# Kernel tuning notes

Measured on AMD Instinct MI355X. Metric: run time of the kernel, lower is better.

## Reference

```python
import jax, jax.numpy as jnp
import numpy as np

H, KVH, P = 32, 8, 64          # heads, kv heads, head_dim (state dim n == P here)
GROUPS = H // KVH
D = H * P                      # hidden = 2048
CONV_DIM = (H + 2 * KVH) * P   # 3072
PROJ = (H + 2 * KVH + H) * P + H  # 5152
CHUNK = 128
EPS = 1e-5
B_, L_ = 2, 2048


def silu(x):
    return x * jax.nn.sigmoid(x)


def segsum(x):
    # x: [..., T] -> [..., T, T] with out[i, j] = sum_{j < k <= i} x[k], -inf above diag
    T = x.shape[-1]
    xb = jnp.broadcast_to(x[..., :, None], x.shape + (T,))
    strict = jnp.tril(jnp.ones((T, T), bool), -1)
    s = jnp.cumsum(jnp.where(strict, xb, 0.0), axis=-2)
    incl = jnp.tril(jnp.ones((T, T), bool))
    return jnp.where(incl, s, -jnp.inf)


def ssd(x, A, Bm, Cm, chunk):
    # Mamba2 chunked scan (SSD). x:[b,l,h,p] (already * dt), A:[b,l,h] (A*dt), B/C:[b,l,h,n]
    b, l, h, p = x.shape
    n = Bm.shape[-1]
    c = l // chunk
    x = x.reshape(b, c, chunk, h, p)
    Bm = Bm.reshape(b, c, chunk, h, n)
    Cm = Cm.reshape(b, c, chunk, h, n)
    A = A.reshape(b, c, chunk, h).transpose(0, 3, 1, 2)  # [b,h,c,l]
    Acs = jnp.cumsum(A, axis=-1)
    # intra-chunk (diagonal blocks)
    Lmat = jnp.exp(segsum(A))  # [b,h,c,l,l]
    Yd = jnp.einsum('bclhn,bcshn,bhcls,bcshp->bclhp', Cm, Bm, Lmat, x)
    # chunk-final states
    dstates = jnp.exp(Acs[..., -1:] - Acs)  # [b,h,c,l]
    states = jnp.einsum('bclhn,bhcl,bclhp->bchpn', Bm, dstates, x)
    states = jnp.concatenate([jnp.zeros_like(states[:, :1]), states], axis=1)
    dchunk = jnp.exp(segsum(jnp.pad(Acs[..., -1], ((0, 0), (0, 0), (1, 0)))))  # [b,h,c+1,c+1]
    states = jnp.einsum('bhzc,bchpn->bzhpn', dchunk, states)[:, :-1]
    # inter-chunk contribution
    Yo = jnp.einsum('bclhn,bchpn,bhcl->bclhp', Cm, states, jnp.exp(Acs))
    return (Yd + Yo).reshape(b, l, h, p)


def setup_inputs() -> dict:
    key = jax.random.key(0)
    ks = jax.random.split(key, 8)
    s = 0.02
    hidden_states = jax.random.normal(ks[0], (B_, L_, D), jnp.float32)
    W_vkqgdt = jax.random.normal(ks[1], (PROJ, D), jnp.float32) * s
    # conv init: identity tap on last position + small noise so grads are nontrivial
    conv_w = jnp.zeros((CONV_DIM, 2), jnp.float32).at[:, 1].set(1.0)
    conv_w = conv_w + jax.random.normal(ks[2], (CONV_DIM, 2), jnp.float32) * s
    conv_b = jax.random.normal(ks[3], (CONV_DIM,), jnp.float32) * s
    # dt_bias init as in the module: inverse-softplus of dt ~ LogUniform(1e-3, 1e-1)
    u = jax.random.uniform(ks[4], (H,), jnp.float32)
    dtv = jnp.exp(u * (np.log(0.1) - np.log(0.001)) + np.log(0.001))
    dtv = jnp.clip(dtv, 0.001)
    dt_bias = dtv + jnp.log(-jnp.expm1(-dtv))
    A_log_bias = jnp.zeros((H,), jnp.float32)
    gnorm_w = jnp.ones((P,), jnp.float32)
    W_o = jax.random.normal(ks[5], (D, D), jnp.float32) * s
    return {'hidden_states': hidden_states, 'W_vkqgdt': W_vkqgdt, 'conv_w': conv_w,
            'conv_b': conv_b, 'dt_bias': dt_bias, 'A_log_bias': A_log_bias,
            'gnorm_w': gnorm_w, 'W_o': W_o}


def reference(hidden_states, W_vkqgdt, conv_w, conv_b, dt_bias, A_log_bias, gnorm_w, W_o):
    b, l, _ = hidden_states.shape
    proj = hidden_states @ W_vkqgdt.T  # [b,l,PROJ]
    vkq, g, dt = jnp.split(proj, [CONV_DIM, CONV_DIM + H * P], axis=2)
    # causal depthwise conv (kernel=2) + SiLU
    x_prev = jnp.pad(vkq, ((0, 0), (1, 0), (0, 0)))[:, :-1]
    vkq = silu(x_prev * conv_w[:, 0] + vkq * conv_w[:, 1] + conv_b)
    v, k, q = jnp.split(vkq, [KVH * P, 2 * KVH * P], axis=2)
    v = jnp.repeat(v.reshape(b, l, KVH, P), GROUPS, axis=2)  # [b,l,H,P]
    k = jnp.repeat(k.reshape(b, l, KVH, P), GROUPS, axis=2)
    q = q.reshape(b, l, H, P)
    dt = jax.nn.softplus(dt + dt_bias)          # [b,l,H]
    A = -jnp.exp(A_log_bias.astype(jnp.float32))  # [H]
    y = ssd(v * dt[..., None], dt * A, k, q, CHUNK)  # x=v, B=k, C=q
    # fused RMSNorm + swish gate
    g = g.reshape(b, l, H, P)
    yn = y * jax.lax.rsqrt(jnp.mean(y * y, axis=-1, keepdims=True) + EPS) * gnorm_w
    y_true = (yn * silu(g)).reshape(b, l, D)
    return y_true @ W_o.T
```

## Files before the change

kernel.cpp:

```cpp
#include <hip/hip_runtime.h>
#include <hip/hip_bf16.h>
#include <math.h>

typedef __bf16 bf16;
typedef __bf16 bf16x4 __attribute__((ext_vector_type(4)));
typedef __bf16 bf16x8 __attribute__((ext_vector_type(8)));
typedef float f32x4 __attribute__((ext_vector_type(4)));

#define NB 2
#define LSEQ 2048
#define NH 32
#define NKVH 8
#define HD 64
#define DMODEL 2048
#define CONVD 3072
#define NPROJ 5152
#define NPADN 5248
#define NCHUNK 16
#define CHUNK 128
#define ROWS 4096
#define EPSF 1e-5f

__device__ __forceinline__ float fsilu(float x) { return x / (1.0f + __expf(-x)); }
__device__ __forceinline__ float fsoftplus(float raw) {
  return (raw > 20.0f) ? raw : log1pf(__expf(raw));
}

__device__ __forceinline__ void gld_lds16(const void* g, void* l) {
  __builtin_amdgcn_global_load_lds(
      (const __attribute__((address_space(1))) void*)g,
      (__attribute__((address_space(3))) void*)l, 16, 0, 0);
}

__device__ __forceinline__ bf16x8 lds_read_b128(const bf16* p) {
  bf16x8 r;
  unsigned off = (unsigned)(unsigned long)(__attribute__((address_space(3))) bf16*)p;
  asm volatile("ds_read_b128 %0, %1" : "=v"(r) : "v"(off));
  return r;
}
#define SBAR() asm volatile("s_barrier" ::: "memory")

__device__ __forceinline__ int swz64(int row, int col) {
  return row * 64 + ((((col >> 3) ^ row) & 7) << 3) + (col & 7);
}
__device__ __forceinline__ int swz128(int row, int col) {
  return row * 128 + (((col >> 3) ^ (row & 7)) << 3) + (col & 7);
}

__device__ __forceinline__ void stage64(const bf16* gsrc, bf16* lds, int tid, int nelem) {
  for (int i0 = 0; i0 < nelem; i0 += 2048) {
    int e = i0 + tid * 8;
    int row = e >> 6;
    int sc = ((tid & 7) ^ (row & 7)) << 3;
    gld_lds16((const void*)(gsrc + (row << 6) + sc), (void*)(lds + e));
  }
}
__device__ __forceinline__ void stage128(const bf16* gsrc, bf16* lds, int tid, int nelem) {
  for (int i0 = 0; i0 < nelem; i0 += 2048) {
    int e = i0 + tid * 8;
    int row = e >> 7;
    int sc = (((tid & 15) ^ (row & 7))) << 3;
    gld_lds16((const void*)(gsrc + (row << 7) + sc), (void*)(lds + e));
  }
}

__device__ __forceinline__ void stage_tileY(const bf16* g, bf16* l, int ldg, int tid) {
#pragma unroll
  for (int it = 0; it < 4; ++it) {
    int e = it * 2048 + tid * 8;
    int r = e >> 6;
    int sc = ((tid & 7) ^ (r & 7)) << 3;
    gld_lds16((const void*)(g + (long)r * ldg + sc), (void*)(l + e));
  }
}

__device__ __forceinline__ void wave_scan128(float& a0, float& a1, int lane) {
#pragma unroll
  for (int off = 1; off < 64; off <<= 1) {
    float t0 = __shfl_up(a0, off);
    float t1 = __shfl_up(a1, off);
    if (lane >= off) { a0 += t0; a1 += t1; }
  }
  a1 += __shfl(a0, 63);
}

__global__ __launch_bounds__(256) void cast_all_kernel(
    const float* __restrict__ hs, const float* __restrict__ w1, const float* __restrict__ wo,
    bf16* __restrict__ hs_b, bf16* __restrict__ w1_b, bf16* __restrict__ wo_b) {
  const long n1 = (long)ROWS * DMODEL / 8;
  const long n2 = (long)NPADN * DMODEL / 8;
  const long n3 = (long)DMODEL * DMODEL / 8;
  long total = n1 + n2 + n3;
  long stride = (long)gridDim.x * blockDim.x;
  for (long i = blockIdx.x * (long)blockDim.x + threadIdx.x; i < total; i += stride) {
    if (i < n1) {
      float4 v0 = ((const float4*)hs)[2 * i];
      float4 v1 = ((const float4*)hs)[2 * i + 1];
      ((bf16x8*)hs_b)[i] = bf16x8{(bf16)v0.x, (bf16)v0.y, (bf16)v0.z, (bf16)v0.w,
                                  (bf16)v1.x, (bf16)v1.y, (bf16)v1.z, (bf16)v1.w};
    } else if (i < n1 + n2) {
      long j = i - n1;
      int n = (int)((j * 8) >> 11);
      bf16x8 o = {};
      if (n < NPROJ) {
        float4 v0 = ((const float4*)w1)[2 * j];
        float4 v1 = ((const float4*)w1)[2 * j + 1];
        o = bf16x8{(bf16)v0.x, (bf16)v0.y, (bf16)v0.z, (bf16)v0.w,
                   (bf16)v1.x, (bf16)v1.y, (bf16)v1.z, (bf16)v1.w};
      }
      ((bf16x8*)w1_b)[j] = o;
    } else {
      long j = i - n1 - n2;
      float4 v0 = ((const float4*)wo)[2 * j];
      float4 v1 = ((const float4*)wo)[2 * j + 1];
      ((bf16x8*)wo_b)[j] = bf16x8{(bf16)v0.x, (bf16)v0.y, (bf16)v0.z, (bf16)v0.w,
                                  (bf16)v1.x, (bf16)v1.y, (bf16)v1.z, (bf16)v1.w};
    }
  }
}

template <typename OutT>
__global__ __launch_bounds__(256, 2) void gemm2p_kernel(
    const bf16* __restrict__ A, const bf16* __restrict__ B, OutT* __restrict__ C,
    int M, int N, int K, int ntx) {
  __shared__ __align__(16) bf16 As[2 * 128 * 64];
  __shared__ __align__(16) bf16 Bs[2 * 128 * 64];
  const int tid = threadIdx.x;
  const int lane = tid & 63;
  const int wave = tid >> 6;
  const int wm = wave >> 1, wn = wave & 1;

  const int GM = 8;
  int lid = blockIdx.x;
  {
    int nwg = gridDim.x;
    int xcd = lid & 7;
    int q = nwg >> 3, r = nwg & 7;
    lid = (xcd < r ? xcd * (q + 1) : r * (q + 1) + (xcd - r) * q) + (lid >> 3);
  }
  int group = GM * ntx;
  int gid = lid / group;
  int rem = lid - gid * group;
  int bm = gid * GM + (rem % GM);
  int bn = rem / GM;

  const bf16* Ag = A + (long)bm * 128 * K;
  const bf16* Bg = B + (long)bn * 128 * K;
  const int NT = K >> 6;

  const int fbA = (wm * 64 + (lane & 15)) * 64 + (((lane >> 4) ^ (lane & 7)) << 3);
  const int fbB = (wn * 64 + (lane & 15)) * 64 + (((lane >> 4) ^ (lane & 7)) << 3);

  f32x4 acc[4][4] = {};

  stage_tileY(Ag, As, K, tid);
  stage_tileY(Bg, Bs, K, tid);
  asm volatile("s_waitcnt vmcnt(0)" ::: "memory");
  SBAR();

  for (int t = 0; t < NT; ++t) {
    const int c = t & 1;
    const bf16* At = As + c * 8192;
    const bf16* Bt = Bs + c * 8192;
    if (t + 1 < NT) {
      stage_tileY(Ag + (t + 1) * 64, As + (c ^ 1) * 8192, K, tid);
      stage_tileY(Bg + (t + 1) * 64, Bs + (c ^ 1) * 8192, K, tid);
    }
    bf16x8 af[4][2], bf_[4][2];
#pragma unroll
    for (int mi = 0; mi < 4; ++mi)
#pragma unroll
      for (int ks = 0; ks < 2; ++ks)
        af[mi][ks] = lds_read_b128(At + ((fbA + mi * 1024) ^ (ks << 5)));
#pragma unroll
    for (int ni = 0; ni < 4; ++ni)
#pragma unroll
      for (int ks = 0; ks < 2; ++ks)
        bf_[ni][ks] = lds_read_b128(Bt + ((fbB + ni * 1024) ^ (ks << 5)));
    asm volatile("s_waitcnt lgkmcnt(0)" ::: "memory");
    __builtin_amdgcn_sched_barrier(0);
    __builtin_amdgcn_s_setprio(1);
#pragma unroll
    for (int mi = 0; mi < 4; ++mi)
#pragma unroll
      for (int ni = 0; ni < 4; ++ni)
#pragma unroll
        for (int ks = 0; ks < 2; ++ks)
          acc[mi][ni] = __builtin_amdgcn_mfma_f32_16x16x32_bf16(af[mi][ks], bf_[ni][ks], acc[mi][ni], 0, 0, 0);
    __builtin_amdgcn_s_setprio(0);
    asm volatile("s_waitcnt vmcnt(0)" ::: "memory");
    SBAR();
  }

#pragma unroll
  for (int mi = 0; mi < 4; ++mi) {
    int rbase = bm * 128 + wm * 64 + mi * 16 + (lane >> 4) * 4;
#pragma unroll
    for (int ni = 0; ni < 4; ++ni) {
      int col = bn * 128 + wn * 64 + ni * 16 + (lane & 15);
#pragma unroll
      for (int r = 0; r < 4; ++r)
        C[(long)(rbase + r) * N + col] = (OutT)acc[mi][ni][r];
    }
  }
}

__global__ __launch_bounds__(256) void prep_kernel(
    const bf16* __restrict__ proj, const float* __restrict__ conv_w,
    const float* __restrict__ conv_b, const float* __restrict__ dt_bias,
    const float* __restrict__ A_log,
    bf16* __restrict__ Kc, bf16* __restrict__ Kt,
    bf16* __restrict__ Vt, float* __restrict__ dtb, float* __restrict__ adtb) {
  __shared__ float tile[128][65];
  int blk = blockIdx.x, tid = threadIdx.x;

  if (blk < 512) {
    int r = blk;
    bool isK = r < 256;
    int rr = isK ? r : r - 256;
    int kvh = rr & 7, c = (rr >> 3) & 15, b = rr >> 7;
    long rowbase = (long)b * LSEQ + c * CHUNK;
    int chb = (isK ? 512 : 0) + kvh * 64;
    int j = tid >> 1, p0 = (tid & 1) * 32;
    const bf16* cur = proj + (rowbase + j) * NPADN;
    bool hp = (c > 0) || (j > 0);
#pragma unroll
    for (int pp = 0; pp < 32; pp += 4) {
      int p = p0 + pp, ch = chb + p;
      bf16x4 cu = *(const bf16x4*)(cur + ch);
      bf16x4 pv = {};
      if (hp) pv = *(const bf16x4*)(cur + ch - NPADN);
      float4 wa = *(const float4*)(conv_w + 2 * ch);
      float4 wb = *(const float4*)(conv_w + 2 * ch + 4);
      float4 bb = *(const float4*)(conv_b + ch);
      tile[j][p + 0] = fsilu((float)pv[0] * wa.x + (float)cu[0] * wa.y + bb.x);
      tile[j][p + 1] = fsilu((float)pv[1] * wa.z + (float)cu[1] * wa.w + bb.y);
      tile[j][p + 2] = fsilu((float)pv[2] * wb.x + (float)cu[2] * wb.y + bb.z);
      tile[j][p + 3] = fsilu((float)pv[3] * wb.z + (float)cu[3] * wb.w + bb.w);
    }
    __syncthreads();
    long tb = (long)rr * 8192;
    if (isK) {
#pragma unroll
      for (int it = 0; it < 8; ++it) {
        int e = it * 1024 + tid * 4;
        int jj = e >> 6, n = e & 63;
        bf16x4 o = {(bf16)tile[jj][n], (bf16)tile[jj][n + 1], (bf16)tile[jj][n + 2], (bf16)tile[jj][n + 3]};
        *(bf16x4*)(Kc + tb + e) = o;
      }
#pragma unroll
      for (int it = 0; it < 8; ++it) {
        int e = it * 1024 + tid * 4;
        int n = e >> 7, jj = e & 127;
        bf16x4 o = {(bf16)tile[jj][n], (bf16)tile[jj + 1][n], (bf16)tile[jj + 2][n], (bf16)tile[jj + 3][n]};
        *(bf16x4*)(Kt + tb + e) = o;
      }
    } else {
#pragma unroll
      for (int it = 0; it < 8; ++it) {
        int e = it * 1024 + tid * 4;
        int n = e >> 7, jj = e & 127;
        bf16x4 o = {(bf16)tile[jj][n], (bf16)tile[jj + 1][n], (bf16)tile[jj + 2][n], (bf16)tile[jj + 3][n]};
        *(bf16x4*)(Vt + tb + e) = o;
      }
    }
  } else {
    int r = blk - 512;
    int c = r & 15, b = r >> 4;
    long rowbase = (long)b * LSEQ + c * CHUNK;
    int j = tid >> 1, h0 = (tid & 1) * 16;
    const bf16* dr = proj + (rowbase + j) * NPADN + (CONVD + DMODEL);
    int obase = (b * 16 + c) * 32;
#pragma unroll
    for (int u = 0; u < 16; ++u) {
      int h = h0 + u;
      float raw = (float)dr[h] + dt_bias[h];
      float dtv = fsoftplus(raw);
      dtb[(long)(obase + h) * 128 + j] = dtv;
      adtb[(long)(obase + h) * 128 + j] = -__expf(A_log[h]) * dtv;
    }
  }
}

__global__ __launch_bounds__(256) void ssd_states_kernel(
    const bf16* __restrict__ Kt, const bf16* __restrict__ Vt,
    const float* __restrict__ dtb, const float* __restrict__ adtb,
    float* __restrict__ states, float* __restrict__ asum) {
  __shared__ __align__(16) bf16 Vs[64 * 128];
  __shared__ __align__(16) bf16 Ks[64 * 128];
  __shared__ float w[CHUNK];
  int bid = blockIdx.x;
  int h = bid & 31, c = (bid >> 5) & 15, b = bid >> 9;
  int kvh = h >> 2;
  int tid = threadIdx.x;
  int lane = tid & 63, wave = tid >> 6;
  long kvb = (long)(((b * 16 + c) * 8) + kvh) * 8192;

  stage128(Vt + kvb, Vs, tid, 8192);
  stage128(Kt + kvb, Ks, tid, 8192);

  float a0 = adtb[(long)bid * 128 + lane];
  float a1 = adtb[(long)bid * 128 + 64 + lane];
  float d0 = dtb[(long)bid * 128 + lane];
  float d1 = dtb[(long)bid * 128 + 64 + lane];
  wave_scan128(a0, a1, lane);
  float atot = __shfl(a1, 63);
  if (wave == 0) {
    w[lane] = d0 * __expf(atot - a0);
    w[64 + lane] = d1 * __expf(atot - a1);
  }
  __syncthreads();

#pragma unroll
  for (int it = 0; it < 4; ++it) {
    int e = it * 2048 + tid * 8;
    int row = e >> 7;
    int j0 = (((tid & 15) ^ (row & 7))) << 3;
    f32x4 wa = *(const f32x4*)(w + j0);
    f32x4 wb = *(const f32x4*)(w + j0 + 4);
    bf16x8 kv = *(const bf16x8*)(Ks + e);
    kv[0] = (bf16)((float)kv[0] * wa[0]); kv[1] = (bf16)((float)kv[1] * wa[1]);
    kv[2] = (bf16)((float)kv[2] * wa[2]); kv[3] = (bf16)((float)kv[3] * wa[3]);
    kv[4] = (bf16)((float)kv[4] * wb[0]); kv[5] = (bf16)((float)kv[5] * wb[1]);
    kv[6] = (bf16)((float)kv[6] * wb[2]); kv[7] = (bf16)((float)kv[7] * wb[3]);
    *(bf16x8*)(Ks + e) = kv;
  }
  __syncthreads();

  f32x4 sacc[4] = {};
#pragma unroll
  for (int ks = 0; ks < CHUNK; ks += 32) {
    bf16x8 af = *(const bf16x8*)(Vs + swz128(wave * 16 + (lane & 15), ks + (lane >> 4) * 8));
    bf16x8 bf_[4];
#pragma unroll
    for (int ni = 0; ni < 4; ++ni)
      bf_[ni] = *(const bf16x8*)(Ks + swz128(ni * 16 + (lane & 15), ks + (lane >> 4) * 8));
#pragma unroll
    for (int ni = 0; ni < 4; ++ni)
      sacc[ni] = __builtin_amdgcn_mfma_f32_16x16x32_bf16(af, bf_[ni], sacc[ni], 0, 0, 0);
  }
  float* sout = states + (long)bid * (HD * HD);
#pragma unroll
  for (int ni = 0; ni < 4; ++ni) {
    int n = ni * 16 + (lane & 15);
#pragma unroll
    for (int r = 0; r < 4; ++r) {
      int p = wave * 16 + (lane >> 4) * 4 + r;
      sout[p * HD + n] = sacc[ni][r];
    }
  }
  if (tid == 0) asum[(b * NH + h) * NCHUNK + c] = atot;
}

__global__ __launch_bounds__(256) void ssd_scan_kernel(
    const float* __restrict__ states, const float* __restrict__ asum,
    bf16* __restrict__ sprevb) {
  int bid = blockIdx.x;
  int s = bid & 7, h = (bid >> 3) & 31, b = bid >> 8;
  int e0 = s * 512 + threadIdx.x;
  int e1 = e0 + 256;
  float S0 = 0.f, S1 = 0.f;
  const float* as = asum + (b * NH + h) * NCHUNK;
  for (int c = 0; c < NCHUNK; ++c) {
    long off = ((long)((b * NCHUNK + c) * NH + h)) * (HD * HD);
    float g = __expf(as[c]);
    sprevb[off + e0] = (bf16)S0;
    sprevb[off + e1] = (bf16)S1;
    S0 = S0 * g + states[off + e0];
    S1 = S1 * g + states[off + e1];
  }
}

__global__ __launch_bounds__(256) void ssd_out_kernel(
    const bf16* __restrict__ Kc, const bf16* __restrict__ Vt,
    const bf16* __restrict__ sprevb, const float* __restrict__ dtb,
    const float* __restrict__ adtb, const bf16* __restrict__ proj,
    const float* __restrict__ conv_w, const float* __restrict__ conv_b,
    const float* __restrict__ gnw, bf16* __restrict__ yg) {
  __shared__ __align__(16) bf16 Qs[128 * 64];
  __shared__ __align__(16) bf16 KVs[128 * 64];
  __shared__ __align__(16) bf16 G[128 * 128];
  __shared__ __align__(16) bf16 Sps[64 * 64];
  __shared__ float acs[CHUNK];
  __shared__ float dts[CHUNK];
  __shared__ float part[CHUNK][2];
  __shared__ float rs_l[CHUNK];

  int bid = blockIdx.x;
  int h = bid & 31, c = (bid >> 5) & 15, b = bid >> 9;
  int kvh = h >> 2;
  int tid = threadIdx.x;
  int lane = tid & 63, wave = tid >> 6;
  int wm = wave >> 1, wn = wave & 1;
  long rowbase = (long)b * LSEQ + c * CHUNK;
  long kvb = (long)(((b * 16 + c) * 8) + kvh) * 8192;

  stage64(Kc + kvb, KVs, tid, 8192);
  stage64(sprevb + (long)bid * 4096, Sps, tid, 4096);

  {
    int j = tid >> 1, p0 = (tid & 1) * 32;
    const bf16* cur = proj + (rowbase + j) * NPADN;
    bool hp = (c > 0) || (j > 0);
    int chb = 1024 + h * 64;
    bf16* qrow = Qs + j * 64;
#pragma unroll
    for (int pp = 0; pp < 32; pp += 4) {
      int p = p0 + pp, ch = chb + p;
      bf16x4 cu = *(const bf16x4*)(cur + ch);
      bf16x4 pv = {};
      if (hp) pv = *(const bf16x4*)(cur + ch - NPADN);
      float4 wa = *(const float4*)(conv_w + 2 * ch);
      float4 wb = *(const float4*)(conv_w + 2 * ch + 4);
      float4 bb = *(const float4*)(conv_b + ch);
      bf16x4 o;
      o[0] = (bf16)fsilu((float)pv[0] * wa.x + (float)cu[0] * wa.y + bb.x);
      o[1] = (bf16)fsilu((float)pv[1] * wa.z + (float)cu[1] * wa.w + bb.y);
      o[2] = (bf16)fsilu((float)pv[2] * wb.x + (float)cu[2] * wb.y + bb.z);
      o[3] = (bf16)fsilu((float)pv[3] * wb.z + (float)cu[3] * wb.w + bb.w);
      *(bf16x4*)(qrow + ((((p >> 3) ^ j) & 7) << 3) + (p & 7)) = o;
    }
  }

  float a0 = adtb[(long)bid * 128 + lane];
  float a1 = adtb[(long)bid * 128 + 64 + lane];
  float d0 = dtb[(long)bid * 128 + lane];
  float d1 = dtb[(long)bid * 128 + 64 + lane];
  wave_scan128(a0, a1, lane);
  if (wave == 0) {
    acs[lane] = a0; acs[64 + lane] = a1;
    dts[lane] = d0; dts[64 + lane] = d1;
  }
  __syncthreads();

  {
    f32x4 gacc[4][4] = {};
#pragma unroll
    for (int ks = 0; ks < HD; ks += 32) {
      bf16x8 af[4], bf_[4];
#pragma unroll
      for (int mi = 0; mi < 4; ++mi)
        af[mi] = *(const bf16x8*)(Qs + swz64(wm * 64 + mi * 16 + (lane & 15), ks + (lane >> 4) * 8));
#pragma unroll
      for (int ni = 0; ni < 4; ++ni)
        bf_[ni] = *(const bf16x8*)(KVs + swz64(wn * 64 + ni * 16 + (lane & 15), ks + (lane >> 4) * 8));
#pragma unroll
      for (int mi = 0; mi < 4; ++mi)
#pragma unroll
        for (int ni = 0; ni < 4; ++ni)
          gacc[mi][ni] = __builtin_amdgcn_mfma_f32_16x16x32_bf16(af[mi], bf_[ni], gacc[mi][ni], 0, 0, 0);
    }
    float aj[4], dj[4];
#pragma unroll
    for (int ni = 0; ni < 4; ++ni) {
      int j = wn * 64 + ni * 16 + (lane & 15);
      aj[ni] = acs[j];
      dj[ni] = dts[j];
    }
#pragma unroll
    for (int mi = 0; mi < 4; ++mi) {
#pragma unroll
      for (int r = 0; r < 4; ++r) {
        int i = wm * 64 + mi * 16 + (lane >> 4) * 4 + r;
        float ai = acs[i];
#pragma unroll
        for (int ni = 0; ni < 4; ++ni) {
          int j = wn * 64 + ni * 16 + (lane & 15);
          float gv = (j <= i) ? gacc[mi][ni][r] * __expf(ai - aj[ni]) * dj[ni] : 0.f;
          G[swz128(i, j)] = (bf16)gv;
        }
      }
    }
  }
  __syncthreads();

  stage128(Vt + kvb, KVs, tid, 8192);
  __syncthreads();

  f32x4 yacc[4][2] = {};
  f32x4 oacc[4][2] = {};
#pragma unroll
  for (int ks = 0; ks < CHUNK; ks += 32) {
    bf16x8 af[4], bf_[2];
#pragma unroll
    for (int mi = 0; mi < 4; ++mi)
      af[mi] = *(const bf16x8*)(G + swz128(wm * 64 + mi * 16 + (lane & 15), ks + (lane >> 4) * 8));
#pragma unroll
    for (int ni = 0; ni < 2; ++ni)
      bf_[ni] = *(const bf16x8*)(KVs + swz128(wn * 32 + ni * 16 + (lane & 15), ks + (lane >> 4) * 8));
#pragma unroll
    for (int mi = 0; mi < 4; ++mi)
#pragma unroll
      for (int ni = 0; ni < 2; ++ni)
        yacc[mi][ni] = __builtin_amdgcn_mfma_f32_16x16x32_bf16(af[mi], bf_[ni], yacc[mi][ni], 0, 0, 0);
  }
#pragma unroll
  for (int ks = 0; ks < HD; ks += 32) {
    bf16x8 af[4], bf_[2];
#pragma unroll
    for (int mi = 0; mi < 4; ++mi)
      af[mi] = *(const bf16x8*)(Qs + swz64(wm * 64 + mi * 16 + (lane & 15), ks + (lane >> 4) * 8));
#pragma unroll
    for (int ni = 0; ni < 2; ++ni)
      bf_[ni] = *(const bf16x8*)(Sps + swz64(wn * 32 + ni * 16 + (lane & 15), ks + (lane >> 4) * 8));
#pragma unroll
    for (int mi = 0; mi < 4; ++mi)
#pragma unroll
      for (int ni = 0; ni < 2; ++ni)
        oacc[mi][ni] = __builtin_amdgcn_mfma_f32_16x16x32_bf16(af[mi], bf_[ni], oacc[mi][ni], 0, 0, 0);
  }

  float yv[4][2][4];
#pragma unroll
  for (int mi = 0; mi < 4; ++mi) {
#pragma unroll
    for (int r = 0; r < 4; ++r) {
      int i = wm * 64 + mi * 16 + (lane >> 4) * 4 + r;
      float ei = __expf(acs[i]);
      float s = 0.f;
#pragma unroll
      for (int ni = 0; ni < 2; ++ni) {
        float v = yacc[mi][ni][r] + ei * oacc[mi][ni][r];
        yv[mi][ni][r] = v;
        s += v * v;
      }
      s += __shfl_xor(s, 1, 64);
      s += __shfl_xor(s, 2, 64);
      s += __shfl_xor(s, 4, 64);
      s += __shfl_xor(s, 8, 64);
      if ((lane & 15) == 0) part[i][wn] = s;
    }
  }
  __syncthreads();

  for (int i0 = 0; i0 < 8192; i0 += 2048) {
    int e = i0 + tid * 8;
    int row = e >> 6;
    int sc = ((tid & 7) ^ (row & 7)) << 3;
    gld_lds16((const void*)(proj + (rowbase + row) * NPADN + CONVD + h * 64 + sc),
              (void*)(KVs + e));
  }
  if (tid < CHUNK) rs_l[tid] = rsqrtf((part[tid][0] + part[tid][1]) * (1.0f / HD) + EPSF);
  __syncthreads();

#pragma unroll
  for (int mi = 0; mi < 4; ++mi) {
#pragma unroll
    for (int r = 0; r < 4; ++r) {
      int i = wm * 64 + mi * 16 + (lane >> 4) * 4 + r;
      long row = rowbase + i;
      float rs = rs_l[i];
#pragma unroll
      for (int ni = 0; ni < 2; ++ni) {
        int p = wn * 32 + ni * 16 + (lane & 15);
        float gval = (float)KVs[swz64(i, p)];
        float val = yv[mi][ni][r] * rs * gnw[p] * fsilu(gval);
        yg[row * (long)DMODEL + h * HD + p] = (bf16)val;
      }
    }
  }
}

extern "C" void kernel_launch(void* const* d_in, const int* in_sizes, int n_in,
                              void* d_out, int out_size, void* d_ws, size_t ws_size,
                              hipStream_t stream) {
  const float* hs      = (const float*)d_in[0];
  const float* W1      = (const float*)d_in[1];
  const float* conv_w  = (const float*)d_in[2];
  const float* conv_b  = (const float*)d_in[3];
  const float* dt_bias = (const float*)d_in[4];
  const float* A_log   = (const float*)d_in[5];
  const float* gnw     = (const float*)d_in[6];
  const float* Wo      = (const float*)d_in[7];

  char* p = (char*)d_ws;
  bf16* hs_b   = (bf16*)p;  p += (long)ROWS * DMODEL * 2;
  bf16* w1_b   = (bf16*)p;  p += (long)NPADN * DMODEL * 2;
  bf16* wo_b   = (bf16*)p;  p += (long)DMODEL * DMODEL * 2;
  bf16* proj   = (bf16*)p;  p += (long)ROWS * NPADN * 2;
  bf16* Kc     = (bf16*)p;  p += (long)256 * 8192 * 2;
  bf16* Kt     = (bf16*)p;  p += (long)256 * 8192 * 2;
  bf16* Vt     = (bf16*)p;  p += (long)256 * 8192 * 2;
  float* dtb   = (float*)p; p += (long)ROWS * NH * 4;
  float* adtb  = (float*)p; p += (long)ROWS * NH * 4;
  float* st    = (float*)p; p += (long)NB * NCHUNK * NH * HD * HD * 4;
  bf16* sprevb = (bf16*)p;  p += (long)NB * NCHUNK * NH * HD * HD * 2;
  float* asum  = (float*)p; p += (long)NB * NH * NCHUNK * 4;
  bf16* yg     = (bf16*)p;  p += (long)ROWS * DMODEL * 2;

  cast_all_kernel<<<4096, 256, 0, stream>>>(hs, W1, Wo, hs_b, w1_b, wo_b);

  gemm2p_kernel<bf16><<<(ROWS / 128) * (NPADN / 128), 256, 0, stream>>>(
      hs_b, w1_b, proj, ROWS, NPADN, DMODEL, NPADN / 128);

  prep_kernel<<<544, 256, 0, stream>>>(proj, conv_w, conv_b, dt_bias, A_log,
                                       Kc, Kt, Vt, dtb, adtb);

  ssd_states_kernel<<<NB * NCHUNK * NH, 256, 0, stream>>>(Kt, Vt, dtb, adtb, st, asum);
  ssd_scan_kernel<<<NB * NH * 8, 256, 0, stream>>>(st, asum, sprevb);
  ssd_out_kernel<<<NB * NCHUNK * NH, 256, 0, stream>>>(
      Kc, Vt, sprevb, dtb, adtb, proj, conv_w, conv_b, gnw, yg);

  gemm2p_kernel<float><<<(ROWS / 128) * (DMODEL / 128), 256, 0, stream>>>(
      yg, wo_b, (float*)d_out, ROWS, DMODEL, DMODEL, DMODEL / 128);
}
```

Baseline: 337.3 us.

## Fuse conv/dt prep with chunk-state computation per KV head

```diff
diff --git a/kernel.cpp b/kernel.cpp
--- a/kernel.cpp
+++ b/kernel.cpp
@@ -205,25 +205,30 @@
   }
 }
 
-__global__ __launch_bounds__(256) void prep_kernel(
+__global__ __launch_bounds__(256) void fused_kvs_kernel(
     const bf16* __restrict__ proj, const float* __restrict__ conv_w,
     const float* __restrict__ conv_b, const float* __restrict__ dt_bias,
     const float* __restrict__ A_log,
-    bf16* __restrict__ Kc, bf16* __restrict__ Kt,
-    bf16* __restrict__ Vt, float* __restrict__ dtb, float* __restrict__ adtb) {
+    bf16* __restrict__ Kc, bf16* __restrict__ Vt,
+    float* __restrict__ dtb, float* __restrict__ adtb,
+    float* __restrict__ states, float* __restrict__ asum) {
   __shared__ float tile[128][65];
+  __shared__ __align__(16) bf16 Ks[64 * 128];
+  __shared__ __align__(16) bf16 Vs[64 * 128];
+  __shared__ float w4[4][128];
+
   int blk = blockIdx.x, tid = threadIdx.x;
-
-  if (blk < 512) {
-    int r = blk;
-    bool isK = r < 256;
-    int rr = isK ? r : r - 256;
-    int kvh = rr & 7, c = (rr >> 3) & 15, b = rr >> 7;
-    long rowbase = (long)b * LSEQ + c * CHUNK;
-    int chb = (isK ? 512 : 0) + kvh * 64;
-    int j = tid >> 1, p0 = (tid & 1) * 32;
-    const bf16* cur = proj + (rowbase + j) * NPADN;
-    bool hp = (c > 0) || (j > 0);
+  int kvh = blk & 7, c = (blk >> 3) & 15, b = blk >> 7;
+  int lane = tid & 63, wave = tid >> 6;
+  long rowbase = (long)b * LSEQ + c * CHUNK;
+  long tb = (long)((b * 16 + c) * 8 + kvh) * 8192;
+
+  int j = tid >> 1, p0 = (tid & 1) * 32;
+  const bf16* cur = proj + (rowbase + j) * NPADN;
+  bool hp = (c > 0) || (j > 0);
+
+  {
+    int chb = 512 + kvh * 64;
 #pragma unroll
     for (int pp = 0; pp < 32; pp += 4) {
       int p = p0 + pp, ch = chb + p;
@@ -238,118 +243,107 @@
       tile[j][p + 2] = fsilu((float)pv[2] * wb.x + (float)cu[2] * wb.y + bb.z);
       tile[j][p + 3] = fsilu((float)pv[3] * wb.z + (float)cu[3] * wb.w + bb.w);
     }
-    __syncthreads();
-    long tb = (long)rr * 8192;
-    if (isK) {
-#pragma unroll
-      for (int it = 0; it < 8; ++it) {
-        int e = it * 1024 + tid * 4;
-        int jj = e >> 6, n = e & 63;
-        bf16x4 o = {(bf16)tile[jj][n], (bf16)tile[jj][n + 1], (bf16)tile[jj][n + 2], (bf16)tile[jj][n + 3]};
-        *(bf16x4*)(Kc + tb + e) = o;
+  }
+  __syncthreads();
+#pragma unroll
+  for (int it = 0; it < 8; ++it) {
+    int e = it * 1024 + tid * 4;
+    int jj = e >> 6, n = e & 63;
+    bf16x4 o = {(bf16)tile[jj][n], (bf16)tile[jj][n + 1], (bf16)tile[jj][n + 2], (bf16)tile[jj][n + 3]};
+    *(bf16x4*)(Kc + tb + e) = o;
+  }
+#pragma unroll
+  for (int it = 0; it < 8; ++it) {
+    int e = it * 1024 + tid * 4;
+    int n = e >> 7, jj = e & 127;
+    bf16x4 o = {(bf16)tile[jj][n], (bf16)tile[jj + 1][n], (bf16)tile[jj + 2][n], (bf16)tile[jj + 3][n]};
+    *(bf16x4*)(Ks + n * 128 + (((jj >> 3) ^ (n & 7)) << 3) + (jj & 7)) = o;
+  }
+  __syncthreads();
+
+  {
+    int chb = kvh * 64;
+#pragma unroll
+    for (int pp = 0; pp < 32; pp += 4) {
+      int p = p0 + pp, ch = chb + p;
+      bf16x4 cu = *(const bf16x4*)(cur + ch);
+      bf16x4 pv = {};
+      if (hp) pv = *(const bf16x4*)(cur + ch - NPADN);
+      float4 wa = *(const float4*)(conv_w + 2 * ch);
+      float4 wb = *(const float4*)(conv_w + 2 * ch + 4);
+      float4 bb = *(const float4*)(conv_b + ch);
+      tile[j][p + 0] = fsilu((float)pv[0] * wa.x + (float)cu[0] * wa.y + bb.x);
+      tile[j][p + 1] = fsilu((float)pv[1] * wa.z + (float)cu[1] * wa.w + bb.y);
+      tile[j][p + 2] = fsilu((float)pv[2] * wb.x + (float)cu[2] * wb.y + bb.z);
+      tile[j][p + 3] = fsilu((float)pv[3] * wb.z + (float)cu[3] * wb.w + bb.w);
+    }
+  }
+  __syncthreads();
+#pragma unroll
+  for (int it = 0; it < 8; ++it) {
+    int e = it * 1024 + tid * 4;
+    int n = e >> 7, jj = e & 127;
+    bf16x4 o = {(bf16)tile[jj][n], (bf16)tile[jj + 1][n], (bf16)tile[jj + 2][n], (bf16)tile[jj + 3][n]};
+    *(bf16x4*)(Vt + tb + e) = o;
+    *(bf16x4*)(Vs + n * 128 + (((jj >> 3) ^ (n & 7)) << 3) + (jj & 7)) = o;
+  }
+
+  int h = kvh * 4 + wave;
+  {
+    const bf16* dr = proj + (rowbase) * NPADN + (CONVD + DMODEL) + h;
+    float raw0 = (float)dr[(long)lane * NPADN] + dt_bias[h];
+    float raw1 = (float)dr[(long)(64 + lane) * NPADN] + dt_bias[h];
+    float dt0 = fsoftplus(raw0), dt1 = fsoftplus(raw1);
+    float mA = -__expf(A_log[h]);
+    float a0 = mA * dt0, a1 = mA * dt1;
+    long dbase = (long)((b * 16 + c) * 32 + h) * 128;
+    dtb[dbase + lane] = dt0; dtb[dbase + 64 + lane] = dt1;
+    adtb[dbase + lane] = a0; adtb[dbase + 64 + lane] = a1;
+    wave_scan128(a0, a1, lane);
+    float atot = __shfl(a1, 63);
+    w4[wave][lane] = dt0 * __expf(atot - a0);
+    w4[wave][64 + lane] = dt1 * __expf(atot - a1);
+    if (lane == 0) asum[(b * NH + h) * NCHUNK + c] = atot;
+  }
+  __syncthreads();
+
+  f32x4 acc[4][4] = {};
+#pragma unroll
+  for (int ks = 0; ks < CHUNK; ks += 32) {
+    int j0 = ks + (lane >> 4) * 8;
+    f32x4 wva = *(const f32x4*)&w4[wave][j0];
+    f32x4 wvb = *(const f32x4*)&w4[wave][j0 + 4];
+    bf16x8 vf[4], kf[4];
+#pragma unroll
+    for (int pi = 0; pi < 4; ++pi)
+      vf[pi] = *(const bf16x8*)(Vs + swz128(pi * 16 + (lane & 15), j0));
+#pragma unroll
+    for (int ni = 0; ni < 4; ++ni) {
+      bf16x8 kv = *(const bf16x8*)(Ks + swz128(ni * 16 + (lane & 15), j0));
+      kv[0] = (bf16)((float)kv[0] * wva[0]); kv[1] = (bf16)((float)kv[1] * wva[1]);
+      kv[2] = (bf16)((float)kv[2] * wva[2]); kv[3] = (bf16)((float)kv[3] * wva[3]);
+      kv[4] = (bf16)((float)kv[4] * wvb[0]); kv[5] = (bf16)((float)kv[5] * wvb[1]);
+      kv[6] = (bf16)((float)kv[6] * wvb[2]); kv[7] = (bf16)((float)kv[7] * wvb[3]);
+      kf[ni] = kv;
+    }
+#pragma unroll
+    for (int pi = 0; pi < 4; ++pi)
+#pragma unroll
+      for (int ni = 0; ni < 4; ++ni)
+        acc[pi][ni] = __builtin_amdgcn_mfma_f32_16x16x32_bf16(vf[pi], kf[ni], acc[pi][ni], 0, 0, 0);
+  }
+  float* sout = states + (long)((b * 16 + c) * 32 + h) * (HD * HD);
+#pragma unroll
+  for (int pi = 0; pi < 4; ++pi)
+#pragma unroll
+    for (int ni = 0; ni < 4; ++ni) {
+      int n = ni * 16 + (lane & 15);
+#pragma unroll
+      for (int r = 0; r < 4; ++r) {
+        int p = pi * 16 + (lane >> 4) * 4 + r;
+        sout[p * HD + n] = acc[pi][ni][r];
       }
-#pragma unroll
-      for (int it = 0; it < 8; ++it) {
-        int e = it * 1024 + tid * 4;
-        int n = e >> 7, jj = e & 127;
-        bf16x4 o = {(bf16)tile[jj][n], (bf16)tile[jj + 1][n], (bf16)tile[jj + 2][n], (bf16)tile[jj + 3][n]};
-        *(bf16x4*)(Kt + tb + e) = o;
-      }
-    } else {
-#pragma unroll
-      for (int it = 0; it < 8; ++it) {
-        int e = it * 1024 + tid * 4;
-        int n = e >> 7, jj = e & 127;
-        bf16x4 o = {(bf16)tile[jj][n], (bf16)tile[jj + 1][n], (bf16)tile[jj + 2][n], (bf16)tile[jj + 3][n]};
-        *(bf16x4*)(Vt + tb + e) = o;
-      }
-    }
-  } else {
-    int r = blk - 512;
-    int c = r & 15, b = r >> 4;
-    long rowbase = (long)b * LSEQ + c * CHUNK;
-    int j = tid >> 1, h0 = (tid & 1) * 16;
-    const bf16* dr = proj + (rowbase + j) * NPADN + (CONVD + DMODEL);
-    int obase = (b * 16 + c) * 32;
-#pragma unroll
-    for (int u = 0; u < 16; ++u) {
-      int h = h0 + u;
-      float raw = (float)dr[h] + dt_bias[h];
-      float dtv = fsoftplus(raw);
-      dtb[(long)(obase + h) * 128 + j] = dtv;
-      adtb[(long)(obase + h) * 128 + j] = -__expf(A_log[h]) * dtv;
-    }
-  }
-}
-
-__global__ __launch_bounds__(256) void ssd_states_kernel(
-    const bf16* __restrict__ Kt, const bf16* __restrict__ Vt,
-    const float* __restrict__ dtb, const float* __restrict__ adtb,
-    float* __restrict__ states, float* __restrict__ asum) {
-  __shared__ __align__(16) bf16 Vs[64 * 128];
-  __shared__ __align__(16) bf16 Ks[64 * 128];
-  __shared__ float w[CHUNK];
-  int bid = blockIdx.x;
-  int h = bid & 31, c = (bid >> 5) & 15, b = bid >> 9;
-  int kvh = h >> 2;
-  int tid = threadIdx.x;
-  int lane = tid & 63, wave = tid >> 6;
-  long kvb = (long)(((b * 16 + c) * 8) + kvh) * 8192;
-
-  stage128(Vt + kvb, Vs, tid, 8192);
-  stage128(Kt + kvb, Ks, tid, 8192);
-
-  float a0 = adtb[(long)bid * 128 + lane];
-  float a1 = adtb[(long)bid * 128 + 64 + lane];
-  float d0 = dtb[(long)bid * 128 + lane];
-  float d1 = dtb[(long)bid * 128 + 64 + lane];
-  wave_scan128(a0, a1, lane);
-  float atot = __shfl(a1, 63);
-  if (wave == 0) {
-    w[lane] = d0 * __expf(atot - a0);
-    w[64 + lane] = d1 * __expf(atot - a1);
-  }
-  __syncthreads();
-
-#pragma unroll
-  for (int it = 0; it < 4; ++it) {
-    int e = it * 2048 + tid * 8;
-    int row = e >> 7;
-    int j0 = (((tid & 15) ^ (row & 7))) << 3;
-    f32x4 wa = *(const f32x4*)(w + j0);
-    f32x4 wb = *(const f32x4*)(w + j0 + 4);
-    bf16x8 kv = *(const bf16x8*)(Ks + e);
-    kv[0] = (bf16)((float)kv[0] * wa[0]); kv[1] = (bf16)((float)kv[1] * wa[1]);
-    kv[2] = (bf16)((float)kv[2] * wa[2]); kv[3] = (bf16)((float)kv[3] * wa[3]);
-    kv[4] = (bf16)((float)kv[4] * wb[0]); kv[5] = (bf16)((float)kv[5] * wb[1]);
-    kv[6] = (bf16)((float)kv[6] * wb[2]); kv[7] = (bf16)((float)kv[7] * wb[3]);
-    *(bf16x8*)(Ks + e) = kv;
-  }
-  __syncthreads();
-
-  f32x4 sacc[4] = {};
-#pragma unroll
-  for (int ks = 0; ks < CHUNK; ks += 32) {
-    bf16x8 af = *(const bf16x8*)(Vs + swz128(wave * 16 + (lane & 15), ks + (lane >> 4) * 8));
-    bf16x8 bf_[4];
-#pragma unroll
-    for (int ni = 0; ni < 4; ++ni)
-      bf_[ni] = *(const bf16x8*)(Ks + swz128(ni * 16 + (lane & 15), ks + (lane >> 4) * 8));
-#pragma unroll
-    for (int ni = 0; ni < 4; ++ni)
-      sacc[ni] = __builtin_amdgcn_mfma_f32_16x16x32_bf16(af, bf_[ni], sacc[ni], 0, 0, 0);
-  }
-  float* sout = states + (long)bid * (HD * HD);
-#pragma unroll
-  for (int ni = 0; ni < 4; ++ni) {
-    int n = ni * 16 + (lane & 15);
-#pragma unroll
-    for (int r = 0; r < 4; ++r) {
-      int p = wave * 16 + (lane >> 4) * 4 + r;
-      sout[p * HD + n] = sacc[ni][r];
-    }
-  }
-  if (tid == 0) asum[(b * NH + h) * NCHUNK + c] = atot;
+    }
 }
 
 __global__ __launch_bounds__(256) void ssd_scan_kernel(
@@ -579,7 +573,6 @@
   bf16* wo_b   = (bf16*)p;  p += (long)DMODEL * DMODEL * 2;
   bf16* proj   = (bf16*)p;  p += (long)ROWS * NPADN * 2;
   bf16* Kc     = (bf16*)p;  p += (long)256 * 8192 * 2;
-  bf16* Kt     = (bf16*)p;  p += (long)256 * 8192 * 2;
   bf16* Vt     = (bf16*)p;  p += (long)256 * 8192 * 2;
   float* dtb   = (float*)p; p += (long)ROWS * NH * 4;
   float* adtb  = (float*)p; p += (long)ROWS * NH * 4;
@@ -593,10 +586,9 @@
   gemm2p_kernel<bf16><<<(ROWS / 128) * (NPADN / 128), 256, 0, stream>>>(
       hs_b, w1_b, proj, ROWS, NPADN, DMODEL, NPADN / 128);
 
-  prep_kernel<<<544, 256, 0, stream>>>(proj, conv_w, conv_b, dt_bias, A_log,
-                                       Kc, Kt, Vt, dtb, adtb);
-
-  ssd_states_kernel<<<NB * NCHUNK * NH, 256, 0, stream>>>(Kt, Vt, dtb, adtb, st, asum);
+  fused_kvs_kernel<<<NB * NCHUNK * NKVH, 256, 0, stream>>>(
+      proj, conv_w, conv_b, dt_bias, A_log, Kc, Vt, dtb, adtb, st, asum);
+
   ssd_scan_kernel<<<NB * NH * 8, 256, 0, stream>>>(st, asum, sprevb);
   ssd_out_kernel<<<NB * NCHUNK * NH, 256, 0, stream>>>(
       Kc, Vt, sprevb, dtb, adtb, proj, conv_w, conv_b, gnw, yg);
```

After: 327.0 us. -3.1%, faster.
